# Kernel tuning notes

Measured on AMD Instinct MI355X. Metric: run time of the kernel, lower is better.

The kernel has to match this reference:

```python
import jax, jax.numpy as jnp
import numpy as np

L = 1024  # seq_len


def setup_inputs() -> dict:
    key = jax.random.key(0)
    ks = jax.random.split(key, 9)
    B = 4
    x = jax.random.uniform(ks[0], (B, L, L), dtype=jnp.float32)          # scores from pre_model
    M = (jax.random.uniform(ks[1], (B, L, L)) < 0.5).astype(jnp.float32)  # pairing-constraint mask
    M = M * M.transpose(0, 2, 1)  # symmetric binary mask
    return {
        "x": x,
        "M": M,
        "s": jnp.float32(0.5),
        "w": jax.random.uniform(ks[2], (1,), dtype=jnp.float32),
        "rho_p": jax.random.uniform(ks[3], (L, L), dtype=jnp.float32),
        "alpha": jnp.float32(0.005),
        "belt": jnp.float32(0.05),
        "lr_alpha": jnp.float32(0.99),
        "lr_belt": jnp.float32(0.99),
        "steps": 16,
    }


def _T_A(A_hat, M):
    # symmetrize then mask
    return (A_hat + A_hat.transpose(0, 2, 1)) * 0.5 * M


def reference(x, M, s, w, rho_p, alpha, belt, lr_alpha, lr_belt, steps):
    scores = x                      # pre_model output, [B, L, L]
    U = scores - s
    A_hat0 = scores
    A0 = _T_A(A_hat0, M)
    Lm0 = w * jax.nn.relu(jnp.sum(A0, axis=-1) - 1.0)   # [B, L] (w broadcasts)

    def step(carry, t):
        Lm, A, A_hat = carry
        # G = U/2 - Lm * sign(rowsum(A) - 1), broadcast over last dim
        row = jnp.sum(A, axis=-1) - 1.0                  # [B, L]
        G = U * 0.5 - (Lm * jnp.sign(row))[:, :, None]   # [B, L, L]
        at = alpha * jnp.power(lr_alpha, t)
        A_hat = A_hat + at * A_hat * M * (G + G.transpose(0, 2, 1))
        A_hat = jax.nn.relu(jnp.abs(A_hat) - rho_p * at)  # soft threshold
        A_hat = 1.0 - jax.nn.relu(1.0 - A_hat)            # clip above at 1
        A = _T_A(A_hat, M)
        Lm = Lm + belt * jnp.power(lr_belt, t) * jax.nn.relu(jnp.sum(A, axis=-1) - 1.0)
        return (Lm, A, A_hat), None

    ts = jnp.arange(steps, dtype=jnp.float32)
    (Lm, A, A_hat), _ = jax.lax.scan(step, (Lm0, A0, A_hat0), ts)
    return A
```

## Files before the change

kernel.cpp:

```cpp
#include <hip/hip_runtime.h>
#include <cstddef>
#include <math.h>

static constexpr int L = 1024;
static constexpr int B = 4;
static constexpr int NSTEPS = 16;
static constexpr int NTILE = 16;
static constexpr int NPAIR = NTILE * (NTILE + 1) / 2;

static constexpr size_t AH_OFF  = 0;
static constexpr size_t US_OFF  = (size_t)B * L * L;
static constexpr size_t CP_OFF  = 2 * (size_t)B * L * L;
static constexpr size_t RP0_OFF = CP_OFF + (size_t)B * 256 * L;
static constexpr size_t CP0_OFF = RP0_OFF + (size_t)B * 16 * L;
static constexpr size_t R_OFF   = CP0_OFF + (size_t)B * 16 * L;
static constexpr size_t LM_OFF  = R_OFF + (size_t)B * L;
static constexpr size_t CC_OFF  = LM_OFF + (size_t)B * L;
static constexpr size_t SC_OFF  = CC_OFF + (size_t)B * L;

__global__ __launch_bounds__(256) void init_kernel(
    const float* __restrict__ x, const float* __restrict__ M,
    const float* __restrict__ sp,
    float* __restrict__ ah, float* __restrict__ us,
    float* __restrict__ Rpart, float* __restrict__ Cpart0)
{
    __shared__ float lt[64][65];
    __shared__ float cpw[4][64];
    const int bid  = blockIdx.x;
    const int chunk = bid & 7;
    const int rest  = bid >> 3;
    const int b  = rest >> 5;
    const int ti = (chunk << 1) | ((rest >> 4) & 1);
    const int tj = rest & 15;
    const int t  = threadIdx.x;
    const int w  = t >> 6;
    const int r  = t >> 4;
    const int c4 = (t & 15) << 2;
    const float s = sp[0];
    const float* xb = x + (size_t)b * L * L;

#pragma unroll
    for (int it = 0; it < 4; ++it) {
        int rr = r + 16 * it;
        float4 v = *(const float4*)(xb + (size_t)(tj * 64 + rr) * L + ti * 64 + c4);
        lt[rr][c4+0] = v.x; lt[rr][c4+1] = v.y; lt[rr][c4+2] = v.z; lt[rr][c4+3] = v.w;
    }
    __syncthreads();

    float cs0 = 0.f, cs1 = 0.f, cs2 = 0.f, cs3 = 0.f;
#pragma unroll
    for (int it = 0; it < 4; ++it) {
        int rr = r + 16 * it;
        int gi = ti * 64 + rr;
        size_t off = (size_t)b * L * L + (size_t)gi * L + tj * 64 + c4;
        float4 xv = *(const float4*)(x + off);
        float4 mv = *(const float4*)(M + off);
        *(float4*)(us + off) = make_float4(0.5f*(xv.x + lt[c4+0][rr]) - s,
                                           0.5f*(xv.y + lt[c4+1][rr]) - s,
                                           0.5f*(xv.z + lt[c4+2][rr]) - s,
                                           0.5f*(xv.w + lt[c4+3][rr]) - s);
        float a0 = xv.x*mv.x, a1 = xv.y*mv.y, a2 = xv.z*mv.z, a3 = xv.w*mv.w;
        *(float4*)(ah + off) = make_float4(a0, a1, a2, a3);
        float rs = (a0 + a1) + (a2 + a3);
        rs += __shfl_xor(rs, 1); rs += __shfl_xor(rs, 2);
        rs += __shfl_xor(rs, 4); rs += __shfl_xor(rs, 8);
        if ((t & 15) == 0) Rpart[((size_t)(b * 16 + tj)) * L + gi] = rs;
        cs0 += a0; cs1 += a1; cs2 += a2; cs3 += a3;
    }
    cs0 += __shfl_xor(cs0, 16); cs0 += __shfl_xor(cs0, 32);
    cs1 += __shfl_xor(cs1, 16); cs1 += __shfl_xor(cs1, 32);
    cs2 += __shfl_xor(cs2, 16); cs2 += __shfl_xor(cs2, 32);
    cs3 += __shfl_xor(cs3, 16); cs3 += __shfl_xor(cs3, 32);
    if ((t & 63) < 16) {
        int c0 = (t & 63) << 2;
        cpw[w][c0+0] = cs0; cpw[w][c0+1] = cs1; cpw[w][c0+2] = cs2; cpw[w][c0+3] = cs3;
    }
    __syncthreads();
    if (t < 64)
        Cpart0[((size_t)(b * 16 + ti)) * L + tj * 64 + t] =
            (cpw[0][t] + cpw[1][t]) + (cpw[2][t] + cpw[3][t]);
}

__global__ __launch_bounds__(256) void lminit_kernel(
    const float* __restrict__ wp,
    const float* __restrict__ alphap, const float* __restrict__ beltp,
    const float* __restrict__ lrap,  const float* __restrict__ lrbp,
    const float* __restrict__ Rpart, const float* __restrict__ Cpart0,
    float* __restrict__ Lm, float* __restrict__ cc, float* __restrict__ sc)
{
    const int bid = blockIdx.x;
    const int t   = threadIdx.x;
    if (bid == 0 && t < NSTEPS) {
        sc[t]          = alphap[0] * powf(lrap[0], (float)t);
        sc[NSTEPS + t] = beltp[0]  * powf(lrbp[0], (float)t);
    }
    const int b   = bid >> 2;
    const int i   = ((bid & 3) << 8) + t;
    float R0 = 0.f, C0 = 0.f;
#pragma unroll
    for (int k = 0; k < 16; ++k) {
        R0 += Rpart[((size_t)(b * 16 + k)) * L + i];
        C0 += Cpart0[((size_t)(b * 16 + k)) * L + i];
    }
    float rowv = 0.5f * (R0 + C0) - 1.0f;
    float rl = fmaxf(rowv, 0.f);
    float lm = wp[0] * rl;
    Lm[b * L + i] = lm;
    float sg = (rowv > 0.f) ? 1.f : ((rowv < 0.f) ? -1.f : 0.f);
    cc[b * L + i] = lm * sg;
}

__device__ __forceinline__ float step_elem(float a, float u, float rho,
                                           float ci, float cj, float at) {
    float g = u - ci - cj;
    float v = a * (1.f + at * g);
    v = fmaxf(fabsf(v) - rho * at, 0.f);
    return fminf(v, 1.f);
}

template <bool DO_SUMS>
__global__ __launch_bounds__(512) void update_kernel(
    const float* __restrict__ rho, const float* __restrict__ sc,
    float* __restrict__ ah, const float* __restrict__ us,
    const float* __restrict__ cc,
    float* __restrict__ R, float* __restrict__ Cpart, int p)
{
    __shared__ float cp[8][1024];
    const int bid   = blockIdx.x;
    const int chunk = bid & 7;
    const int rest  = bid >> 3;
    const int b     = rest >> 4;
    const int slab  = (chunk << 4) | (rest & 15);
    const int t    = threadIdx.x;
    const int w    = t >> 6;
    const int l    = t & 63;
    const int row  = (slab << 3) + w;
    const size_t rowoff = (size_t)b * L * L + (size_t)row * L;
    const float at = sc[p];
    const float* ccb = cc + b * L;

    float4 cj[4];
#pragma unroll
    for (int k = 0; k < 4; ++k)
        cj[k] = *(const float4*)(ccb + k * 256 + l * 4);
    const float ci = ccb[row];

    float4 a4[4], u4[4], h4[4];
#pragma unroll
    for (int k = 0; k < 4; ++k) {
        const size_t off = rowoff + k * 256 + l * 4;
        a4[k] = *(const float4*)(ah + off);
        u4[k] = *(const float4*)(us + off);
        h4[k] = *(const float4*)(rho + (size_t)row * L + k * 256 + l * 4);
    }
#pragma unroll
    for (int k = 0; k < 4; ++k) {
        a4[k].x = step_elem(a4[k].x, u4[k].x, h4[k].x, ci, cj[k].x, at);
        a4[k].y = step_elem(a4[k].y, u4[k].y, h4[k].y, ci, cj[k].y, at);
        a4[k].z = step_elem(a4[k].z, u4[k].z, h4[k].z, ci, cj[k].z, at);
        a4[k].w = step_elem(a4[k].w, u4[k].w, h4[k].w, ci, cj[k].w, at);
        *(float4*)(ah + rowoff + k * 256 + l * 4) = a4[k];
    }

    if (DO_SUMS) {
        float rs = 0.f;
#pragma unroll
        for (int k = 0; k < 4; ++k)
            rs += (a4[k].x + a4[k].y) + (a4[k].z + a4[k].w);
        rs += __shfl_xor(rs, 1);  rs += __shfl_xor(rs, 2);  rs += __shfl_xor(rs, 4);
        rs += __shfl_xor(rs, 8);  rs += __shfl_xor(rs, 16); rs += __shfl_xor(rs, 32);
        if (l == 0) R[b * L + row] = rs;

#pragma unroll
        for (int k = 0; k < 4; ++k)
            *(float4*)&cp[w][k * 256 + l * 4] = a4[k];
        __syncthreads();
        const int c0 = t * 2;
        float2 acc = make_float2(0.f, 0.f);
#pragma unroll
        for (int j = 0; j < 8; ++j) {
            float2 v = *(float2*)&cp[j][c0];
            acc.x += v.x; acc.y += v.y;
        }
        *(float2*)(Cpart + ((size_t)(b * 128 + slab)) * L + c0) = acc;
    }
}

__global__ __launch_bounds__(1024) void lmreduce_kernel(
    const float* __restrict__ sc,
    const float* __restrict__ Cpart, const float* __restrict__ R,
    float* __restrict__ Lm, float* __restrict__ cc, int p)
{
    __shared__ float red[16][64];
    const int bid = blockIdx.x;
    const int b   = bid >> 4;
    const int c0  = (bid & 15) << 6;
    const int t   = threadIdx.x;
    const int w   = t >> 6;
    const int l   = t & 63;
    const int c   = c0 + l;

    const float* base = Cpart + (size_t)b * 128 * L + c;
    float v = 0.f;
#pragma unroll
    for (int k = w * 8; k < w * 8 + 8; ++k)
        v += base[(size_t)k * L];
    red[w][l] = v;
    __syncthreads();

    if (w == 0) {
        float total = 0.f;
#pragma unroll
        for (int j = 0; j < 16; ++j) total += red[j][l];
        float rowv = 0.5f * (R[b * L + c] + total) - 1.0f;
        float rl = fmaxf(rowv, 0.f);
        float lm = Lm[b * L + c] + sc[NSTEPS + p] * rl;
        Lm[b * L + c] = lm;
        float sg = (rowv > 0.f) ? 1.f : ((rowv < 0.f) ? -1.f : 0.f);
        cc[b * L + c] = lm * sg;
    }
}

__device__ __forceinline__ void decode_pair(int p, int& ti, int& tj) {
    int t = 0;
    while (p >= NTILE - t) { p -= NTILE - t; ++t; }
    ti = t; tj = t + p;
}

__global__ __launch_bounds__(256) void final_kernel(
    const float* __restrict__ ah, float* __restrict__ out)
{
    __shared__ float la[64][65];
    __shared__ float lb[64][65];
    const int task = blockIdx.x;
    const int b = task / NPAIR;
    int ti, tj; decode_pair(task % NPAIR, ti, tj);
    const int t  = threadIdx.x;
    const int r0 = t >> 4;
    const int c0 = (t & 15) << 2;
    const float* ahb = ah  + (size_t)b * L * L;
    float* ob        = out + (size_t)b * L * L;

    for (int it = 0; it < 4; ++it) {
        int r = r0 + 16 * it;
        float4 va = *(const float4*)(ahb + (size_t)(ti * 64 + r) * L + tj * 64 + c0);
        la[r][c0+0] = va.x; la[r][c0+1] = va.y; la[r][c0+2] = va.z; la[r][c0+3] = va.w;
        if (ti != tj) {
            float4 vb = *(const float4*)(ahb + (size_t)(tj * 64 + r) * L + ti * 64 + c0);
            lb[r][c0+0] = vb.x; lb[r][c0+1] = vb.y; lb[r][c0+2] = vb.z; lb[r][c0+3] = vb.w;
        }
    }
    __syncthreads();

    for (int it = 0; it < 4; ++it) {
        int r = r0 + 16 * it;
        size_t off = (size_t)(ti * 64 + r) * L + tj * 64 + c0;
        float tb0, tb1, tb2, tb3;
        if (ti == tj) { tb0 = la[c0+0][r]; tb1 = la[c0+1][r]; tb2 = la[c0+2][r]; tb3 = la[c0+3][r]; }
        else          { tb0 = lb[c0+0][r]; tb1 = lb[c0+1][r]; tb2 = lb[c0+2][r]; tb3 = lb[c0+3][r]; }
        *(float4*)(ob + off) = make_float4(0.5f*(la[r][c0+0]+tb0), 0.5f*(la[r][c0+1]+tb1),
                                           0.5f*(la[r][c0+2]+tb2), 0.5f*(la[r][c0+3]+tb3));
    }
    if (ti != tj) {
        for (int it = 0; it < 4; ++it) {
            int r = r0 + 16 * it;
            size_t off = (size_t)(tj * 64 + r) * L + ti * 64 + c0;
            *(float4*)(ob + off) = make_float4(0.5f*(lb[r][c0+0]+la[c0+0][r]),
                                               0.5f*(lb[r][c0+1]+la[c0+1][r]),
                                               0.5f*(lb[r][c0+2]+la[c0+2][r]),
                                               0.5f*(lb[r][c0+3]+la[c0+3][r]));
        }
    }
}

extern "C" void kernel_launch(void* const* d_in, const int* in_sizes, int n_in,
                              void* d_out, int out_size, void* d_ws, size_t ws_size,
                              hipStream_t stream) {
    const float* x     = (const float*)d_in[0];
    const float* M     = (const float*)d_in[1];
    const float* s     = (const float*)d_in[2];
    const float* w     = (const float*)d_in[3];
    const float* rho   = (const float*)d_in[4];
    const float* alpha = (const float*)d_in[5];
    const float* belt  = (const float*)d_in[6];
    const float* lra   = (const float*)d_in[7];
    const float* lrb   = (const float*)d_in[8];
    float* out = (float*)d_out;

    float* ws     = (float*)d_ws;
    float* ah     = ws + AH_OFF;
    float* us     = ws + US_OFF;
    float* Cpart  = ws + CP_OFF;
    float* Rpart  = ws + RP0_OFF;
    float* Cpart0 = ws + CP0_OFF;
    float* R      = ws + R_OFF;
    float* Lm     = ws + LM_OFF;
    float* cc     = ws + CC_OFF;
    float* sc     = ws + SC_OFF;

    init_kernel<<<dim3(1024), dim3(256), 0, stream>>>(x, M, s, ah, us, Rpart, Cpart0);
    lminit_kernel<<<dim3(16), dim3(256), 0, stream>>>(
        w, alpha, belt, lra, lrb, Rpart, Cpart0, Lm, cc, sc);
    for (int p = 0; p < NSTEPS; ++p) {
        if (p < NSTEPS - 1) {
            update_kernel<true><<<dim3(512), dim3(512), 0, stream>>>(
                rho, sc, ah, us, cc, R, Cpart, p);
            lmreduce_kernel<<<dim3(64), dim3(1024), 0, stream>>>(
                sc, Cpart, R, Lm, cc, p);
        } else {
            update_kernel<false><<<dim3(512), dim3(512), 0, stream>>>(
                rho, sc, ah, us, cc, R, Cpart, p);
        }
    }
    final_kernel<<<dim3(B * NPAIR), dim3(256), 0, stream>>>(ah, out);
}
```

Before: 279.8 us.

## Fuse all iteration steps into one cooperative persistent kernel with grid sync

Replaces the 31 per-step update and reduction kernel launches with one cooperative kernel. In it, each block keeps its 16 rows of A_hat, U and rho in registers across all steps and does a grid-wide sync between steps. Column sums are accumulated with fixed-point 64-bit atomics and row sums are written per step, so every block can recompute Lm and the correction terms locally. This removes launch overhead and the per-step global re-reads and re-writes of A_hat and U. In exchange it needs 256 co-resident blocks of 1024 threads and pays for grid syncs and atomics. If the cooperative launch fails, it falls back to the old per-step path.

```diff
diff --git a/kernel.cpp b/kernel.cpp
--- a/kernel.cpp
+++ b/kernel.cpp
@@ -1,12 +1,16 @@
 #include <hip/hip_runtime.h>
+#include <hip/hip_cooperative_groups.h>
 #include <cstddef>
 #include <math.h>
+
+namespace cg = cooperative_groups;
 
 static constexpr int L = 1024;
 static constexpr int B = 4;
 static constexpr int NSTEPS = 16;
 static constexpr int NTILE = 16;
 static constexpr int NPAIR = NTILE * (NTILE + 1) / 2;
+static constexpr int BL = B * L;
 
 static constexpr size_t AH_OFF  = 0;
 static constexpr size_t US_OFF  = (size_t)B * L * L;
@@ -17,16 +21,23 @@
 static constexpr size_t LM_OFF  = R_OFF + (size_t)B * L;
 static constexpr size_t CC_OFF  = LM_OFF + (size_t)B * L;
 static constexpr size_t SC_OFF  = CC_OFF + (size_t)B * L;
+static constexpr size_t RS_OFF  = SC_OFF + 64;
+static constexpr size_t CS_OFF  = RS_OFF + (size_t)(NSTEPS - 1) * BL;
 
 __global__ __launch_bounds__(256) void init_kernel(
     const float* __restrict__ x, const float* __restrict__ M,
     const float* __restrict__ sp,
     float* __restrict__ ah, float* __restrict__ us,
-    float* __restrict__ Rpart, float* __restrict__ Cpart0)
+    float* __restrict__ Rpart, float* __restrict__ Cpart0,
+    unsigned long long* __restrict__ Cs)
 {
     __shared__ float lt[64][65];
     __shared__ float cpw[4][64];
     const int bid  = blockIdx.x;
+    {
+        const int gid = bid * 256 + threadIdx.x;
+        if (gid < (NSTEPS - 1) * BL) Cs[gid] = 0ull;
+    }
     const int chunk = bid & 7;
     const int rest  = bid >> 3;
     const int b  = rest >> 5;
@@ -118,6 +129,99 @@
     return fminf(v, 1.f);
 }
 
+__global__ __launch_bounds__(1024, 4) void steps_kernel(
+    const float* __restrict__ rho, const float* __restrict__ sc,
+    float* __restrict__ ah, const float* __restrict__ us,
+    const float* __restrict__ Lm0, const float* __restrict__ cc0,
+    float* __restrict__ Rs, unsigned long long* __restrict__ Cs)
+{
+    cg::grid_group grid = cg::this_grid();
+    __shared__ float cc_lds[1024];
+    __shared__ float lm_lds[1024];
+    __shared__ float cp[8][1024];
+
+    const int t    = threadIdx.x;
+    const int w    = t >> 6;
+    const int l    = t & 63;
+    const int bid  = blockIdx.x;
+    const int b    = bid >> 6;
+    const int slab = bid & 63;
+    const int row  = (slab << 4) | w;
+    const size_t rowoff = (size_t)b * L * L + (size_t)row * L;
+
+    cc_lds[t] = cc0[b * L + t];
+    lm_lds[t] = Lm0[b * L + t];
+
+    float4 a4[4], u4[4], h4[4];
+#pragma unroll
+    for (int k = 0; k < 4; ++k) {
+        const size_t off = rowoff + (k << 8) + (l << 2);
+        a4[k] = *(const float4*)(ah + off);
+        u4[k] = *(const float4*)(us + off);
+        h4[k] = *(const float4*)(rho + (size_t)row * L + (k << 8) + (l << 2));
+    }
+    __syncthreads();
+
+    for (int p = 0; p < NSTEPS; ++p) {
+        const float at = sc[p];
+        const float ci = cc_lds[row];
+        float rs = 0.f;
+#pragma unroll
+        for (int k = 0; k < 4; ++k) {
+            float4 c4 = *(const float4*)&cc_lds[(k << 8) + (l << 2)];
+            a4[k].x = step_elem(a4[k].x, u4[k].x, h4[k].x, ci, c4.x, at);
+            a4[k].y = step_elem(a4[k].y, u4[k].y, h4[k].y, ci, c4.y, at);
+            a4[k].z = step_elem(a4[k].z, u4[k].z, h4[k].z, ci, c4.z, at);
+            a4[k].w = step_elem(a4[k].w, u4[k].w, h4[k].w, ci, c4.w, at);
+            rs += (a4[k].x + a4[k].y) + (a4[k].z + a4[k].w);
+        }
+        if (p == NSTEPS - 1) break;
+
+        rs += __shfl_xor(rs, 1);  rs += __shfl_xor(rs, 2);  rs += __shfl_xor(rs, 4);
+        rs += __shfl_xor(rs, 8);  rs += __shfl_xor(rs, 16); rs += __shfl_xor(rs, 32);
+        if (l == 0) Rs[(size_t)p * BL + b * L + row] = rs;
+
+        if (w >= 8) {
+#pragma unroll
+            for (int k = 0; k < 4; ++k)
+                *(float4*)&cp[w - 8][(k << 8) + (l << 2)] = a4[k];
+        }
+        __syncthreads();
+        if (w < 8) {
+#pragma unroll
+            for (int k = 0; k < 4; ++k) {
+                float4* q = (float4*)&cp[w][(k << 8) + (l << 2)];
+                float4 v = *q;
+                v.x += a4[k].x; v.y += a4[k].y; v.z += a4[k].z; v.w += a4[k].w;
+                *q = v;
+            }
+        }
+        __syncthreads();
+        float csum = 0.f;
+#pragma unroll
+        for (int j = 0; j < 8; ++j) csum += cp[j][t];
+        atomicAdd(Cs + (size_t)p * BL + b * L + t,
+                  (unsigned long long)((double)csum * 4294967296.0));
+
+        grid.sync();
+
+        {
+            float Cv = (float)((double)Cs[(size_t)p * BL + b * L + t] *
+                               (1.0 / 4294967296.0));
+            float Rv = Rs[(size_t)p * BL + b * L + t];
+            float rowv = 0.5f * (Rv + Cv) - 1.0f;
+            float lm = lm_lds[t] + sc[NSTEPS + p] * fmaxf(rowv, 0.f);
+            lm_lds[t] = lm;
+            cc_lds[t] = lm * ((rowv > 0.f) ? 1.f : ((rowv < 0.f) ? -1.f : 0.f));
+        }
+        __syncthreads();
+    }
+
+#pragma unroll
+    for (int k = 0; k < 4; ++k)
+        *(float4*)(ah + rowoff + (k << 8) + (l << 2)) = a4[k];
+}
+
 template <bool DO_SUMS>
 __global__ __launch_bounds__(512) void update_kernel(
     const float* __restrict__ rho, const float* __restrict__ sc,
@@ -297,20 +401,35 @@
     float* Lm     = ws + LM_OFF;
     float* cc     = ws + CC_OFF;
     float* sc     = ws + SC_OFF;
-
-    init_kernel<<<dim3(1024), dim3(256), 0, stream>>>(x, M, s, ah, us, Rpart, Cpart0);
+    float* Rs     = ws + RS_OFF;
+    unsigned long long* Cs = (unsigned long long*)(ws + CS_OFF);
+
+    init_kernel<<<dim3(1024), dim3(256), 0, stream>>>(x, M, s, ah, us, Rpart, Cpart0, Cs);
     lminit_kernel<<<dim3(16), dim3(256), 0, stream>>>(
         w, alpha, belt, lra, lrb, Rpart, Cpart0, Lm, cc, sc);
-    for (int p = 0; p < NSTEPS; ++p) {
-        if (p < NSTEPS - 1) {
-            update_kernel<true><<<dim3(512), dim3(512), 0, stream>>>(
-                rho, sc, ah, us, cc, R, Cpart, p);
-            lmreduce_kernel<<<dim3(64), dim3(1024), 0, stream>>>(
-                sc, Cpart, R, Lm, cc, p);
-        } else {
-            update_kernel<false><<<dim3(512), dim3(512), 0, stream>>>(
-                rho, sc, ah, us, cc, R, Cpart, p);
-        }
-    }
+
+    {
+        const float* rho_ = rho; const float* sc_ = sc;
+        float* ah_ = ah; const float* us_ = us;
+        const float* Lm_ = Lm; const float* cc_ = cc;
+        float* Rs_ = Rs; unsigned long long* Cs_ = Cs;
+        void* args[] = { &rho_, &sc_, &ah_, &us_, &Lm_, &cc_, &Rs_, &Cs_ };
+        hipError_t err = hipLaunchCooperativeKernel(
+            (void*)steps_kernel, dim3(B * 64), dim3(1024), args, 0, stream);
+        if (err != hipSuccess) {
+            for (int p = 0; p < NSTEPS; ++p) {
+                if (p < NSTEPS - 1) {
+                    update_kernel<true><<<dim3(512), dim3(512), 0, stream>>>(
+                        rho, sc, ah, us, cc, R, Cpart, p);
+                    lmreduce_kernel<<<dim3(64), dim3(1024), 0, stream>>>(
+                        sc, Cpart, R, Lm, cc, p);
+                } else {
+                    update_kernel<false><<<dim3(512), dim3(512), 0, stream>>>(
+                        rho, sc, ah, us, cc, R, Cpart, p);
+                }
+            }
+        }
+    }
+
     final_kernel<<<dim3(B * NPAIR), dim3(256), 0, stream>>>(ah, out);
 }
```

Measured after the change: 559.1 us. +99.8%, slower.

## Fuse Lagrange-multiplier reduction into update kernel via fixed-point atomic accumulation

Applied to the files above, without the earlier changes.

Drops the separate lmreduce kernel. Each update kernel now atomically accumulates row and column sums into banked 64-bit fixed-point buffers, one per step. The next step's update kernel reduces the banks itself to recompute Lm and the sign term into LDS. This removes 15 kernel launches and the large partial-sum write and re-read. The cost is global atomics, redundant Lm recomputation in every block, fixed-point rounding, and zeroing the atomic buffers in init.

```diff
diff --git a/kernel.cpp b/kernel.cpp
--- a/kernel.cpp
+++ b/kernel.cpp
@@ -7,26 +7,34 @@
 static constexpr int NSTEPS = 16;
 static constexpr int NTILE = 16;
 static constexpr int NPAIR = NTILE * (NTILE + 1) / 2;
+static constexpr int BL = B * L;
+static constexpr int NBANK = 4;
 
 static constexpr size_t AH_OFF  = 0;
 static constexpr size_t US_OFF  = (size_t)B * L * L;
-static constexpr size_t CP_OFF  = 2 * (size_t)B * L * L;
-static constexpr size_t RP0_OFF = CP_OFF + (size_t)B * 256 * L;
+static constexpr size_t RP0_OFF = 2 * (size_t)B * L * L;
 static constexpr size_t CP0_OFF = RP0_OFF + (size_t)B * 16 * L;
-static constexpr size_t R_OFF   = CP0_OFF + (size_t)B * 16 * L;
-static constexpr size_t LM_OFF  = R_OFF + (size_t)B * L;
-static constexpr size_t CC_OFF  = LM_OFF + (size_t)B * L;
-static constexpr size_t SC_OFF  = CC_OFF + (size_t)B * L;
+static constexpr size_t LMA_OFF = CP0_OFF + (size_t)B * 16 * L;
+static constexpr size_t LMB_OFF = LMA_OFF + (size_t)BL;
+static constexpr size_t CC0_OFF = LMB_OFF + (size_t)BL;
+static constexpr size_t SC_OFF  = CC0_OFF + (size_t)BL;
+static constexpr size_t CS_OFF  = SC_OFF + 64;
+static constexpr size_t CS_U64  = (size_t)(NSTEPS - 1) * NBANK * BL;
 
 __global__ __launch_bounds__(256) void init_kernel(
     const float* __restrict__ x, const float* __restrict__ M,
     const float* __restrict__ sp,
     float* __restrict__ ah, float* __restrict__ us,
-    float* __restrict__ Rpart, float* __restrict__ Cpart0)
+    float* __restrict__ Rpart, float* __restrict__ Cpart0,
+    unsigned long long* __restrict__ Cs)
 {
     __shared__ float lt[64][65];
     __shared__ float cpw[4][64];
     const int bid  = blockIdx.x;
+    {
+        const size_t gid = (size_t)bid * 256 + threadIdx.x;
+        if (gid < CS_U64) Cs[gid] = 0ull;
+    }
     const int chunk = bid & 7;
     const int rest  = bid >> 3;
     const int b  = rest >> 5;
@@ -86,7 +94,7 @@
     const float* __restrict__ alphap, const float* __restrict__ beltp,
     const float* __restrict__ lrap,  const float* __restrict__ lrbp,
     const float* __restrict__ Rpart, const float* __restrict__ Cpart0,
-    float* __restrict__ Lm, float* __restrict__ cc, float* __restrict__ sc)
+    float* __restrict__ Lm0, float* __restrict__ cc0, float* __restrict__ sc)
 {
     const int bid = blockIdx.x;
     const int t   = threadIdx.x;
@@ -105,9 +113,9 @@
     float rowv = 0.5f * (R0 + C0) - 1.0f;
     float rl = fmaxf(rowv, 0.f);
     float lm = wp[0] * rl;
-    Lm[b * L + i] = lm;
+    Lm0[b * L + i] = lm;
     float sg = (rowv > 0.f) ? 1.f : ((rowv < 0.f) ? -1.f : 0.f);
-    cc[b * L + i] = lm * sg;
+    cc0[b * L + i] = lm * sg;
 }
 
 __device__ __forceinline__ float step_elem(float a, float u, float rho,
@@ -118,13 +126,15 @@
     return fminf(v, 1.f);
 }
 
-template <bool DO_SUMS>
+template <bool DO_SUMS, bool FIRST>
 __global__ __launch_bounds__(512) void update_kernel(
     const float* __restrict__ rho, const float* __restrict__ sc,
     float* __restrict__ ah, const float* __restrict__ us,
-    const float* __restrict__ cc,
-    float* __restrict__ R, float* __restrict__ Cpart, int p)
+    const float* __restrict__ cc0,
+    const float* __restrict__ lm_in, float* __restrict__ lm_out,
+    unsigned long long* __restrict__ Cs, int p)
 {
+    __shared__ float cc_lds[1024];
     __shared__ float cp[8][1024];
     const int bid   = blockIdx.x;
     const int chunk = bid & 7;
@@ -137,13 +147,6 @@
     const int row  = (slab << 3) + w;
     const size_t rowoff = (size_t)b * L * L + (size_t)row * L;
     const float at = sc[p];
-    const float* ccb = cc + b * L;
-
-    float4 cj[4];
-#pragma unroll
-    for (int k = 0; k < 4; ++k)
-        cj[k] = *(const float4*)(ccb + k * 256 + l * 4);
-    const float ci = ccb[row];
 
     float4 a4[4], u4[4], h4[4];
 #pragma unroll
@@ -153,23 +156,50 @@
         u4[k] = *(const float4*)(us + off);
         h4[k] = *(const float4*)(rho + (size_t)row * L + k * 256 + l * 4);
     }
+
+    if (FIRST) {
+        cc_lds[t]       = cc0[b * L + t];
+        cc_lds[t + 512] = cc0[b * L + t + 512];
+    } else {
+        const float bp = sc[NSTEPS + p - 1];
+#pragma unroll
+        for (int h = 0; h < 2; ++h) {
+            const int c = t + h * 512;
+            const size_t cbase = ((size_t)(p - 1) * NBANK) * BL + b * L + c;
+            unsigned long long craw = 0ull;
+#pragma unroll
+            for (int q = 0; q < NBANK; ++q)
+                craw += Cs[cbase + (size_t)q * BL];
+            float rowv = (float)((double)craw * (1.0 / 4294967296.0)) - 1.0f;
+            float lm = lm_in[b * L + c] + bp * fmaxf(rowv, 0.f);
+            if (slab == 0) lm_out[b * L + c] = lm;
+            cc_lds[c] = lm * ((rowv > 0.f) ? 1.f : ((rowv < 0.f) ? -1.f : 0.f));
+        }
+    }
+    __syncthreads();
+
+    const float ci = cc_lds[row];
+    float rs = 0.f;
 #pragma unroll
     for (int k = 0; k < 4; ++k) {
-        a4[k].x = step_elem(a4[k].x, u4[k].x, h4[k].x, ci, cj[k].x, at);
-        a4[k].y = step_elem(a4[k].y, u4[k].y, h4[k].y, ci, cj[k].y, at);
-        a4[k].z = step_elem(a4[k].z, u4[k].z, h4[k].z, ci, cj[k].z, at);
-        a4[k].w = step_elem(a4[k].w, u4[k].w, h4[k].w, ci, cj[k].w, at);
+        float4 c4 = *(const float4*)&cc_lds[k * 256 + l * 4];
+        a4[k].x = step_elem(a4[k].x, u4[k].x, h4[k].x, ci, c4.x, at);
+        a4[k].y = step_elem(a4[k].y, u4[k].y, h4[k].y, ci, c4.y, at);
+        a4[k].z = step_elem(a4[k].z, u4[k].z, h4[k].z, ci, c4.z, at);
+        a4[k].w = step_elem(a4[k].w, u4[k].w, h4[k].w, ci, c4.w, at);
+        rs += (a4[k].x + a4[k].y) + (a4[k].z + a4[k].w);
         *(float4*)(ah + rowoff + k * 256 + l * 4) = a4[k];
     }
 
     if (DO_SUMS) {
-        float rs = 0.f;
-#pragma unroll
-        for (int k = 0; k < 4; ++k)
-            rs += (a4[k].x + a4[k].y) + (a4[k].z + a4[k].w);
+        const int bank = slab & (NBANK - 1);
+        const size_t cslice = ((size_t)(p * NBANK + bank)) * BL + b * L;
+
         rs += __shfl_xor(rs, 1);  rs += __shfl_xor(rs, 2);  rs += __shfl_xor(rs, 4);
         rs += __shfl_xor(rs, 8);  rs += __shfl_xor(rs, 16); rs += __shfl_xor(rs, 32);
-        if (l == 0) R[b * L + row] = rs;
+        if (l == 0)
+            atomicAdd(Cs + cslice + row,
+                      (unsigned long long)((double)(0.5f * rs) * 4294967296.0));
 
 #pragma unroll
         for (int k = 0; k < 4; ++k)
@@ -182,42 +212,10 @@
             float2 v = *(float2*)&cp[j][c0];
             acc.x += v.x; acc.y += v.y;
         }
-        *(float2*)(Cpart + ((size_t)(b * 128 + slab)) * L + c0) = acc;
-    }
-}
-
-__global__ __launch_bounds__(1024) void lmreduce_kernel(
-    const float* __restrict__ sc,
-    const float* __restrict__ Cpart, const float* __restrict__ R,
-    float* __restrict__ Lm, float* __restrict__ cc, int p)
-{
-    __shared__ float red[16][64];
-    const int bid = blockIdx.x;
-    const int b   = bid >> 4;
-    const int c0  = (bid & 15) << 6;
-    const int t   = threadIdx.x;
-    const int w   = t >> 6;
-    const int l   = t & 63;
-    const int c   = c0 + l;
-
-    const float* base = Cpart + (size_t)b * 128 * L + c;
-    float v = 0.f;
-#pragma unroll
-    for (int k = w * 8; k < w * 8 + 8; ++k)
-        v += base[(size_t)k * L];
-    red[w][l] = v;
-    __syncthreads();
-
-    if (w == 0) {
-        float total = 0.f;
-#pragma unroll
-        for (int j = 0; j < 16; ++j) total += red[j][l];
-        float rowv = 0.5f * (R[b * L + c] + total) - 1.0f;
-        float rl = fmaxf(rowv, 0.f);
-        float lm = Lm[b * L + c] + sc[NSTEPS + p] * rl;
-        Lm[b * L + c] = lm;
-        float sg = (rowv > 0.f) ? 1.f : ((rowv < 0.f) ? -1.f : 0.f);
-        cc[b * L + c] = lm * sg;
+        atomicAdd(Cs + cslice + c0,
+                  (unsigned long long)((double)(0.5f * acc.x) * 4294967296.0));
+        atomicAdd(Cs + cslice + c0 + 1,
+                  (unsigned long long)((double)(0.5f * acc.y) * 4294967296.0));
     }
 }
 
@@ -290,27 +288,26 @@
     float* ws     = (float*)d_ws;
     float* ah     = ws + AH_OFF;
     float* us     = ws + US_OFF;
-    float* Cpart  = ws + CP_OFF;
     float* Rpart  = ws + RP0_OFF;
     float* Cpart0 = ws + CP0_OFF;
-    float* R      = ws + R_OFF;
-    float* Lm     = ws + LM_OFF;
-    float* cc     = ws + CC_OFF;
+    float* lmbuf[2] = { ws + LMA_OFF, ws + LMB_OFF };
+    float* cc0    = ws + CC0_OFF;
     float* sc     = ws + SC_OFF;
-
-    init_kernel<<<dim3(1024), dim3(256), 0, stream>>>(x, M, s, ah, us, Rpart, Cpart0);
+    unsigned long long* Cs = (unsigned long long*)(ws + CS_OFF);
+
+    init_kernel<<<dim3(1024), dim3(256), 0, stream>>>(x, M, s, ah, us, Rpart, Cpart0, Cs);
     lminit_kernel<<<dim3(16), dim3(256), 0, stream>>>(
-        w, alpha, belt, lra, lrb, Rpart, Cpart0, Lm, cc, sc);
-    for (int p = 0; p < NSTEPS; ++p) {
-        if (p < NSTEPS - 1) {
-            update_kernel<true><<<dim3(512), dim3(512), 0, stream>>>(
-                rho, sc, ah, us, cc, R, Cpart, p);
-            lmreduce_kernel<<<dim3(64), dim3(1024), 0, stream>>>(
-                sc, Cpart, R, Lm, cc, p);
-        } else {
-            update_kernel<false><<<dim3(512), dim3(512), 0, stream>>>(
-                rho, sc, ah, us, cc, R, Cpart, p);
-        }
-    }
+        w, alpha, belt, lra, lrb, Rpart, Cpart0, lmbuf[0], cc0, sc);
+
+    update_kernel<true, true><<<dim3(512), dim3(512), 0, stream>>>(
+        rho, sc, ah, us, cc0, nullptr, nullptr, Cs, 0);
+    for (int p = 1; p < NSTEPS - 1; ++p) {
+        update_kernel<true, false><<<dim3(512), dim3(512), 0, stream>>>(
+            rho, sc, ah, us, cc0, lmbuf[(p - 1) & 1], lmbuf[p & 1], Cs, p);
+    }
+    update_kernel<false, false><<<dim3(512), dim3(512), 0, stream>>>(
+        rho, sc, ah, us, cc0, lmbuf[(NSTEPS - 2) & 1], lmbuf[(NSTEPS - 1) & 1],
+        Cs, NSTEPS - 1);
+
     final_kernel<<<dim3(B * NPAIR), dim3(256), 0, stream>>>(ah, out);
 }
```

Result: slower. 358.8 us (+28.2%).

## Fuse Lagrange reduction into update kernel via atomic counters and fold last step into final

Applied to the files above, without the earlier changes.

Removes the separate lmreduce kernel launch per step. Each update block publishes its row and column partial sums atomically and bumps a per-group counter, and a designated block per column group spin-waits on a root counter before reducing the partials and writing double-buffered Lm/cc for the next step. The last update step is merged into the final symmetrize kernel, which saves one full pass over A_hat. The cost is spin-waiting that assumes the designated blocks' producers are co-resident, which risks stalls if residency does not hold, plus extra reads of U and rho in the final kernel.

```diff
diff --git a/kernel.cpp b/kernel.cpp
--- a/kernel.cpp
+++ b/kernel.cpp
@@ -7,26 +7,36 @@
 static constexpr int NSTEPS = 16;
 static constexpr int NTILE = 16;
 static constexpr int NPAIR = NTILE * (NTILE + 1) / 2;
+static constexpr int BL = B * L;
 
 static constexpr size_t AH_OFF  = 0;
 static constexpr size_t US_OFF  = (size_t)B * L * L;
 static constexpr size_t CP_OFF  = 2 * (size_t)B * L * L;
-static constexpr size_t RP0_OFF = CP_OFF + (size_t)B * 256 * L;
+static constexpr size_t RP0_OFF = CP_OFF + (size_t)B * 128 * L;
 static constexpr size_t CP0_OFF = RP0_OFF + (size_t)B * 16 * L;
 static constexpr size_t R_OFF   = CP0_OFF + (size_t)B * 16 * L;
-static constexpr size_t LM_OFF  = R_OFF + (size_t)B * L;
-static constexpr size_t CC_OFF  = LM_OFF + (size_t)B * L;
-static constexpr size_t SC_OFF  = CC_OFF + (size_t)B * L;
+static constexpr size_t LMA_OFF = R_OFF + (size_t)BL;
+static constexpr size_t LMB_OFF = LMA_OFF + (size_t)BL;
+static constexpr size_t CCA_OFF = LMB_OFF + (size_t)BL;
+static constexpr size_t CCB_OFF = CCA_OFF + (size_t)BL;
+static constexpr size_t SC_OFF  = CCB_OFF + (size_t)BL;
+static constexpr size_t CTR_OFF = SC_OFF + 64;
+static constexpr size_t CTR_U64 = 544;
 
 __global__ __launch_bounds__(256) void init_kernel(
     const float* __restrict__ x, const float* __restrict__ M,
     const float* __restrict__ sp,
     float* __restrict__ ah, float* __restrict__ us,
-    float* __restrict__ Rpart, float* __restrict__ Cpart0)
+    float* __restrict__ Rpart, float* __restrict__ Cpart0,
+    unsigned long long* __restrict__ ctr64)
 {
     __shared__ float lt[64][65];
     __shared__ float cpw[4][64];
     const int bid  = blockIdx.x;
+    {
+        const size_t gid = (size_t)bid * 256 + threadIdx.x;
+        if (gid < CTR_U64) ctr64[gid] = 0ull;
+    }
     const int chunk = bid & 7;
     const int rest  = bid >> 3;
     const int b  = rest >> 5;
@@ -86,7 +96,7 @@
     const float* __restrict__ alphap, const float* __restrict__ beltp,
     const float* __restrict__ lrap,  const float* __restrict__ lrbp,
     const float* __restrict__ Rpart, const float* __restrict__ Cpart0,
-    float* __restrict__ Lm, float* __restrict__ cc, float* __restrict__ sc)
+    float* __restrict__ Lm0, float* __restrict__ cc0, float* __restrict__ sc)
 {
     const int bid = blockIdx.x;
     const int t   = threadIdx.x;
@@ -105,9 +115,9 @@
     float rowv = 0.5f * (R0 + C0) - 1.0f;
     float rl = fmaxf(rowv, 0.f);
     float lm = wp[0] * rl;
-    Lm[b * L + i] = lm;
+    Lm0[b * L + i] = lm;
     float sg = (rowv > 0.f) ? 1.f : ((rowv < 0.f) ? -1.f : 0.f);
-    cc[b * L + i] = lm * sg;
+    cc0[b * L + i] = lm * sg;
 }
 
 __device__ __forceinline__ float step_elem(float a, float u, float rho,
@@ -122,8 +132,11 @@
 __global__ __launch_bounds__(512) void update_kernel(
     const float* __restrict__ rho, const float* __restrict__ sc,
     float* __restrict__ ah, const float* __restrict__ us,
-    const float* __restrict__ cc,
-    float* __restrict__ R, float* __restrict__ Cpart, int p)
+    const float* __restrict__ cc_in,
+    const float* __restrict__ lm_in, float* __restrict__ lm_out,
+    float* __restrict__ cc_out,
+    float* __restrict__ Cpart, float* __restrict__ Rrow,
+    unsigned int* __restrict__ ctr, int p)
 {
     __shared__ float cp[8][1024];
     const int bid   = blockIdx.x;
@@ -137,7 +150,7 @@
     const int row  = (slab << 3) + w;
     const size_t rowoff = (size_t)b * L * L + (size_t)row * L;
     const float at = sc[p];
-    const float* ccb = cc + b * L;
+    const float* ccb = cc_in + b * L;
 
     float4 cj[4];
 #pragma unroll
@@ -169,7 +182,9 @@
             rs += (a4[k].x + a4[k].y) + (a4[k].z + a4[k].w);
         rs += __shfl_xor(rs, 1);  rs += __shfl_xor(rs, 2);  rs += __shfl_xor(rs, 4);
         rs += __shfl_xor(rs, 8);  rs += __shfl_xor(rs, 16); rs += __shfl_xor(rs, 32);
-        if (l == 0) R[b * L + row] = rs;
+        if (l == 0)
+            __hip_atomic_store(&Rrow[b * L + row], rs,
+                               __ATOMIC_RELAXED, __HIP_MEMORY_SCOPE_AGENT);
 
 #pragma unroll
         for (int k = 0; k < 4; ++k)
@@ -182,42 +197,66 @@
             float2 v = *(float2*)&cp[j][c0];
             acc.x += v.x; acc.y += v.y;
         }
-        *(float2*)(Cpart + ((size_t)(b * 128 + slab)) * L + c0) = acc;
-    }
-}
-
-__global__ __launch_bounds__(1024) void lmreduce_kernel(
-    const float* __restrict__ sc,
-    const float* __restrict__ Cpart, const float* __restrict__ R,
-    float* __restrict__ Lm, float* __restrict__ cc, int p)
-{
-    __shared__ float red[16][64];
-    const int bid = blockIdx.x;
-    const int b   = bid >> 4;
-    const int c0  = (bid & 15) << 6;
-    const int t   = threadIdx.x;
-    const int w   = t >> 6;
-    const int l   = t & 63;
-    const int c   = c0 + l;
-
-    const float* base = Cpart + (size_t)b * 128 * L + c;
-    float v = 0.f;
-#pragma unroll
-    for (int k = w * 8; k < w * 8 + 8; ++k)
-        v += base[(size_t)k * L];
-    red[w][l] = v;
-    __syncthreads();
-
-    if (w == 0) {
-        float total = 0.f;
-#pragma unroll
-        for (int j = 0; j < 16; ++j) total += red[j][l];
-        float rowv = 0.5f * (R[b * L + c] + total) - 1.0f;
-        float rl = fmaxf(rowv, 0.f);
-        float lm = Lm[b * L + c] + sc[NSTEPS + p] * rl;
-        Lm[b * L + c] = lm;
-        float sg = (rowv > 0.f) ? 1.f : ((rowv < 0.f) ? -1.f : 0.f);
-        cc[b * L + c] = lm * sg;
+        {
+            unsigned long long* cp64 =
+                (unsigned long long*)(Cpart + ((size_t)(b * 128 + slab)) * L);
+            union { float2 f; unsigned long long u; } pk; pk.f = acc;
+            __hip_atomic_store(&cp64[t], pk.u,
+                               __ATOMIC_RELAXED, __HIP_MEMORY_SCOPE_AGENT);
+        }
+
+        __syncthreads();
+        const int rgrp = slab >> 3;
+        unsigned int* gctr = ctr + ((b << 4) | rgrp) * 16;
+        unsigned int* root = ctr + 1024 + (b << 4);
+        if (t == 0) {
+            unsigned old = __hip_atomic_fetch_add(gctr, 1u, __ATOMIC_RELAXED,
+                                                  __HIP_MEMORY_SCOPE_AGENT);
+            if (old == (unsigned)(p * 8 + 7))
+                __hip_atomic_fetch_add(root, 1u, __ATOMIC_RELAXED,
+                                       __HIP_MEMORY_SCOPE_AGENT);
+        }
+
+        if ((slab & 7) == 0) {
+            if (t == 0) {
+                const unsigned target = (unsigned)(p + 1) * 16u;
+                while (__hip_atomic_load(root, __ATOMIC_RELAXED,
+                                         __HIP_MEMORY_SCOPE_AGENT) < target)
+                    __builtin_amdgcn_s_sleep(1);
+            }
+            __syncthreads();
+            const int i  = slab >> 3;
+            const int g  = t >> 5;
+            const int cpair = t & 31;
+            float sx = 0.f, sy = 0.f;
+#pragma unroll
+            for (int k = g * 8; k < g * 8 + 8; ++k) {
+                const unsigned long long* q =
+                    (const unsigned long long*)(Cpart + ((size_t)(b * 128 + k)) * L);
+                unsigned long long raw = __hip_atomic_load(
+                    &q[i * 32 + cpair], __ATOMIC_RELAXED, __HIP_MEMORY_SCOPE_AGENT);
+                union { unsigned long long u; float2 f; } pk; pk.u = raw;
+                sx += pk.f.x; sy += pk.f.y;
+            }
+            float* red = &cp[0][0];
+            red[g * 64 + cpair * 2]     = sx;
+            red[g * 64 + cpair * 2 + 1] = sy;
+            __syncthreads();
+            if (t < 64) {
+                float tot = 0.f;
+#pragma unroll
+                for (int g2 = 0; g2 < 16; ++g2) tot += red[g2 * 64 + t];
+                const int col = i * 64 + t;
+                float Rv = __hip_atomic_load(&Rrow[b * L + col],
+                                             __ATOMIC_RELAXED,
+                                             __HIP_MEMORY_SCOPE_AGENT);
+                float rowv = 0.5f * (Rv + tot) - 1.0f;
+                float lm = lm_in[b * L + col] + sc[NSTEPS + p] * fmaxf(rowv, 0.f);
+                lm_out[b * L + col] = lm;
+                cc_out[b * L + col] =
+                    lm * ((rowv > 0.f) ? 1.f : ((rowv < 0.f) ? -1.f : 0.f));
+            }
+        }
     }
 }
 
@@ -227,27 +266,58 @@
     ti = t; tj = t + p;
 }
 
-__global__ __launch_bounds__(256) void final_kernel(
-    const float* __restrict__ ah, float* __restrict__ out)
+__global__ __launch_bounds__(256) void updfinal_kernel(
+    const float* __restrict__ rho, const float* __restrict__ sc,
+    const float* __restrict__ ah, const float* __restrict__ us,
+    const float* __restrict__ ccf, float* __restrict__ out)
 {
     __shared__ float la[64][65];
     __shared__ float lb[64][65];
+    __shared__ float uu[64][65];
     const int task = blockIdx.x;
     const int b = task / NPAIR;
     int ti, tj; decode_pair(task % NPAIR, ti, tj);
     const int t  = threadIdx.x;
     const int r0 = t >> 4;
     const int c0 = (t & 15) << 2;
+    const float at = sc[NSTEPS - 1];
+    const float* ccb = ccf + b * L;
     const float* ahb = ah  + (size_t)b * L * L;
+    const float* usb = us  + (size_t)b * L * L;
     float* ob        = out + (size_t)b * L * L;
 
-    for (int it = 0; it < 4; ++it) {
-        int r = r0 + 16 * it;
-        float4 va = *(const float4*)(ahb + (size_t)(ti * 64 + r) * L + tj * 64 + c0);
-        la[r][c0+0] = va.x; la[r][c0+1] = va.y; la[r][c0+2] = va.z; la[r][c0+3] = va.w;
-        if (ti != tj) {
-            float4 vb = *(const float4*)(ahb + (size_t)(tj * 64 + r) * L + ti * 64 + c0);
-            lb[r][c0+0] = vb.x; lb[r][c0+1] = vb.y; lb[r][c0+2] = vb.z; lb[r][c0+3] = vb.w;
+    {
+        float4 cjv = *(const float4*)(ccb + tj * 64 + c0);
+        for (int it = 0; it < 4; ++it) {
+            int r = r0 + 16 * it;
+            int gi = ti * 64 + r;
+            size_t off = (size_t)gi * L + tj * 64 + c0;
+            float4 av = *(const float4*)(ahb + off);
+            float4 uv = *(const float4*)(usb + off);
+            float4 hv = *(const float4*)(rho + off);
+            float ci = ccb[gi];
+            la[r][c0+0] = step_elem(av.x, uv.x, hv.x, ci, cjv.x, at);
+            la[r][c0+1] = step_elem(av.y, uv.y, hv.y, ci, cjv.y, at);
+            la[r][c0+2] = step_elem(av.z, uv.z, hv.z, ci, cjv.z, at);
+            la[r][c0+3] = step_elem(av.w, uv.w, hv.w, ci, cjv.w, at);
+            uu[r][c0+0] = uv.x; uu[r][c0+1] = uv.y;
+            uu[r][c0+2] = uv.z; uu[r][c0+3] = uv.w;
+        }
+    }
+    __syncthreads();
+    if (ti != tj) {
+        float4 cjv = *(const float4*)(ccb + ti * 64 + c0);
+        for (int it = 0; it < 4; ++it) {
+            int r = r0 + 16 * it;
+            int gi = tj * 64 + r;
+            size_t off = (size_t)gi * L + ti * 64 + c0;
+            float4 av = *(const float4*)(ahb + off);
+            float4 hv = *(const float4*)(rho + off);
+            float ci = ccb[gi];
+            lb[r][c0+0] = step_elem(av.x, uu[c0+0][r], hv.x, ci, cjv.x, at);
+            lb[r][c0+1] = step_elem(av.y, uu[c0+1][r], hv.y, ci, cjv.y, at);
+            lb[r][c0+2] = step_elem(av.z, uu[c0+2][r], hv.z, ci, cjv.z, at);
+            lb[r][c0+3] = step_elem(av.w, uu[c0+3][r], hv.w, ci, cjv.w, at);
         }
     }
     __syncthreads();
@@ -293,24 +363,22 @@
     float* Cpart  = ws + CP_OFF;
     float* Rpart  = ws + RP0_OFF;
     float* Cpart0 = ws + CP0_OFF;
-    float* R      = ws + R_OFF;
-    float* Lm     = ws + LM_OFF;
-    float* cc     = ws + CC_OFF;
+    float* Rrow   = ws + R_OFF;
+    float* Lmb[2] = { ws + LMA_OFF, ws + LMB_OFF };
+    float* ccb2[2] = { ws + CCA_OFF, ws + CCB_OFF };
     float* sc     = ws + SC_OFF;
-
-    init_kernel<<<dim3(1024), dim3(256), 0, stream>>>(x, M, s, ah, us, Rpart, Cpart0);
+    unsigned int* ctr = (unsigned int*)(ws + CTR_OFF);
+
+    init_kernel<<<dim3(1024), dim3(256), 0, stream>>>(
+        x, M, s, ah, us, Rpart, Cpart0, (unsigned long long*)ctr);
     lminit_kernel<<<dim3(16), dim3(256), 0, stream>>>(
-        w, alpha, belt, lra, lrb, Rpart, Cpart0, Lm, cc, sc);
-    for (int p = 0; p < NSTEPS; ++p) {
-        if (p < NSTEPS - 1) {
-            update_kernel<true><<<dim3(512), dim3(512), 0, stream>>>(
-                rho, sc, ah, us, cc, R, Cpart, p);
-            lmreduce_kernel<<<dim3(64), dim3(1024), 0, stream>>>(
-                sc, Cpart, R, Lm, cc, p);
-        } else {
-            update_kernel<false><<<dim3(512), dim3(512), 0, stream>>>(
-                rho, sc, ah, us, cc, R, Cpart, p);
-        }
-    }
-    final_kernel<<<dim3(B * NPAIR), dim3(256), 0, stream>>>(ah, out);
-}
+        w, alpha, belt, lra, lrb, Rpart, Cpart0, Lmb[0], ccb2[0], sc);
+
+    for (int p = 0; p < NSTEPS - 1; ++p) {
+        update_kernel<true><<<dim3(512), dim3(512), 0, stream>>>(
+            rho, sc, ah, us, ccb2[p & 1], Lmb[p & 1], Lmb[(p + 1) & 1],
+            ccb2[(p + 1) & 1], Cpart, Rrow, ctr, p);
+    }
+    updfinal_kernel<<<dim3(B * NPAIR), dim3(256), 0, stream>>>(
+        rho, sc, ah, us, ccb2[(NSTEPS - 1) & 1], out);
+}
```

Measured after the change: 302.4 us. 1.08x slower.
